# Kernel tuning notes

Hardware: AMD Instinct MI355X
Metric: run time of the kernel (lower is better)

The kernel has to match this reference:

```python
import jax, jax.numpy as jnp
import numpy as np

N, E, H, IN, OUT, A, L = 20000, 320000, 128, 16, 16, 4, 4
EPS = 1e-5


def _ln(x, g, b):
    mu = jnp.mean(x, axis=-1, keepdims=True)
    v = jnp.mean((x - mu) ** 2, axis=-1, keepdims=True)
    return (x - mu) * jax.lax.rsqrt(v + EPS) * g + b


def setup_inputs() -> dict:
    key = jax.random.key(0)
    ks = jax.random.split(key, 24)
    x = jax.random.normal(ks[0], (N, 3), dtype=jnp.float32)
    h = jax.random.normal(ks[1], (N, IN), dtype=jnp.float32)
    src = jax.random.randint(ks[2], (E,), 0, N)
    src = src.at[:N].set(jnp.arange(N))  # ensure every node has out-degree>=1 so c>0
    dst = jax.random.randint(ks[3], (E,), 0, N)
    edges = jnp.stack([src, dst]).astype(jnp.int32)
    edge_attr = jax.random.normal(ks[4], (E, A), dtype=jnp.float32)
    s = 0.05
    d_in = 2 * H + 1 + A
    p = {
        "emb_w": jax.random.normal(ks[5], (IN, H)) * s, "emb_b": jnp.zeros((H,)),
        "out_w": jax.random.normal(ks[6], (H, OUT)) * s, "out_b": jnp.zeros((OUT,)),
        "pe_w1": jax.random.normal(ks[7], (L, d_in, H)) * s, "pe_b1": jnp.zeros((L, H)),
        "pe_g1": jnp.ones((L, H)), "pe_bb1": jnp.zeros((L, H)),
        "pe_w2": jax.random.normal(ks[8], (L, H, H)) * s, "pe_b2": jnp.zeros((L, H)),
        "pe_g2": jnp.ones((L, H)), "pe_bb2": jnp.zeros((L, H)),
        "px_w1": jax.random.normal(ks[9], (L, H, H)) * s, "px_b1": jnp.zeros((L, H)),
        "px_g1": jnp.ones((L, H)), "px_bb1": jnp.zeros((L, H)),
        "px_w2": jax.random.normal(ks[10], (L, H, 1)) * s, "px_b2": jnp.zeros((L, 1)),
        "ph_w1": jax.random.normal(ks[11], (L, 2 * H, H)) * s, "ph_b1": jnp.zeros((L, H)),
        "ph_g1": jnp.ones((L, H)), "ph_bb1": jnp.zeros((L, H)),
        "ph_w2": jax.random.normal(ks[12], (L, H, H)) * s, "ph_b2": jnp.zeros((L, H)),
    }
    out = {"x": x, "h": h, "edges": edges, "edge_attr": edge_attr}
    out.update(p)
    return out


def reference(x, h, edges, edge_attr, emb_w, emb_b, out_w, out_b,
              pe_w1, pe_b1, pe_g1, pe_bb1, pe_w2, pe_b2, pe_g2, pe_bb2,
              px_w1, px_b1, px_g1, px_bb1, px_w2, px_b2,
              ph_w1, ph_b1, ph_g1, ph_bb1, ph_w2, ph_b2):
    n = x.shape[0]
    j, i = edges[0], edges[1]  # PyG: x_j = source, x_i = target; aggregate at target i
    # c = in-neighborhood size computed from edge_index[0] (as in the original code)
    c = jax.ops.segment_sum(jnp.ones((edges.shape[1],), x.dtype), j, num_segments=n)[:, None]
    h = h @ emb_w + emb_b
    for l in range(L):
        d = x[i] - x[j]                                   # [E,3]
        d2 = jnp.sum(d * d, axis=-1, keepdims=True)       # ||x_i - x_j||^2
        m_in = jnp.concatenate([h[i], h[j], d2, edge_attr], axis=-1)
        t = jax.nn.silu(_ln(m_in @ pe_w1[l] + pe_b1[l], pe_g1[l], pe_bb1[l]))
        mh = jax.nn.silu(_ln(t @ pe_w2[l] + pe_b2[l], pe_g2[l], pe_bb2[l]))  # [E,H]
        t2 = jax.nn.silu(_ln(mh @ px_w1[l] + px_b1[l], px_g1[l], px_bb1[l]))
        mx = d * (t2 @ px_w2[l] + px_b2[l])               # [E,3]
        agg_x = jax.ops.segment_sum(mx, i, num_segments=n)
        agg_h = jax.ops.segment_sum(mh, i, num_segments=n)
        u = jnp.concatenate([h, agg_h], axis=-1)
        t3 = jax.nn.silu(_ln(u @ ph_w1[l] + ph_b1[l], ph_g1[l], ph_bb1[l]))
        h = t3 @ ph_w2[l] + ph_b2[l] + h                  # ResWrapper residual
        x = x + agg_x / c
    h = h @ out_w + out_b
    return (x, h)
```

## Files before the change

kernel.cpp:

```cpp
#include <hip/hip_runtime.h>
#include <hip/hip_bf16.h>

#define NN 20000
#define NE 320000
#define HD 128
#define IND 16
#define OUTD 16
#define NL 4
#define LN_EPS 1e-5f
#define LDA 136

typedef __attribute__((ext_vector_type(8))) short bf16x8;
typedef __attribute__((ext_vector_type(4))) float f32x4;

__device__ __forceinline__ unsigned short f2b(float f) {
  __hip_bfloat16 h = __float2bfloat16(f);
  unsigned short u;
  __builtin_memcpy(&u, &h, 2);
  return u;
}
__device__ __forceinline__ float b2f(unsigned int lo16) {
  union { unsigned int u; float f; } v; v.u = lo16 << 16; return v.f;
}


__global__ void prep_zero_k(const float* __restrict__ xin, float* __restrict__ xf,
                            float* __restrict__ cnt, int* __restrict__ deg) {
  int i = blockIdx.x * 256 + threadIdx.x;
  if (i < NN * 3) xf[i] = xin[i];
  if (i < NN) { cnt[i] = 0.f; deg[i] = 0; }
}

__global__ void count_k(const int* __restrict__ edges, float* __restrict__ cnt,
                        int* __restrict__ deg) {
  int e = blockIdx.x * 256 + threadIdx.x;
  if (e < NE) {
    atomicAdd(&cnt[edges[e]], 1.f);
    atomicAdd(&deg[edges[NE + e]], 1);
  }
}

__global__ void inv_k(float* __restrict__ cnt) {
  int n = blockIdx.x * 256 + threadIdx.x;
  if (n < NN) { float c = cnt[n]; cnt[n] = (c > 0.f) ? 1.f / c : 0.f; }
}

__global__ void scan_k(const int* __restrict__ deg, int* __restrict__ rowptr,
                       int* __restrict__ cursor) {
  __shared__ int part[256];
  const int tid = threadIdx.x;
  const int base = tid * 79;
  int s = 0;
  for (int t = 0; t < 79; ++t) { int idx = base + t; if (idx < NN) s += deg[idx]; }
  part[tid] = s;
  __syncthreads();
  for (int off = 1; off < 256; off <<= 1) {
    int v = (tid >= off) ? part[tid - off] : 0;
    __syncthreads();
    part[tid] += v;
    __syncthreads();
  }
  int run = (tid == 0) ? 0 : part[tid - 1];
  for (int t = 0; t < 79; ++t) {
    int idx = base + t;
    if (idx < NN) { rowptr[idx] = run; cursor[idx] = run; run += deg[idx]; }
  }
  if (tid == 255) rowptr[NN] = run;
}

__global__ void scatter_k(const int* __restrict__ edges, int* __restrict__ cursor,
                          int* __restrict__ eids) {
  int e = blockIdx.x * 256 + threadIdx.x;
  if (e < NE) {
    int d = edges[NE + e];
    int pos = atomicAdd(&cursor[d], 1);
    eids[pos] = e;
  }
}

__global__ void prep_w_k(const float* __restrict__ src, unsigned short* __restrict__ dst,
                         int KT, int Kreal) {
  int i = blockIdx.x * 256 + threadIdx.x;
  int total = NL * KT * 4096;
  if (i >= total) return;
  int kk = i & 31;
  int c = (i >> 5) & 127;
  int lkt = i >> 12;
  int kt = lkt % KT;
  int l = lkt / KT;
  int k = kt * 32 + kk;
  float v = (k < Kreal) ? src[((size_t)l * Kreal + k) * HD + c] : 0.f;
  dst[i] = f2b(v);
}

__global__ void emb_k(const float* __restrict__ hin, const float* __restrict__ w,
                      const float* __restrict__ b, float* __restrict__ hf,
                      unsigned short* __restrict__ hb) {
  int i = blockIdx.x * 256 + threadIdx.x;
  if (i >= NN * HD) return;
  int n = i >> 7, c = i & 127;
  float acc = b[c];
#pragma unroll
  for (int k = 0; k < IND; ++k) acc += hin[n * IND + k] * w[k * HD + c];
  hf[i] = acc;
  hb[i] = f2b(acc);
}

__global__ void prepd_k(const float* __restrict__ xf, const int* __restrict__ edges,
                        const float* __restrict__ ea, float* __restrict__ dvec,
                        unsigned short* __restrict__ e8) {
  int e = blockIdx.x * 256 + threadIdx.x;
  if (e >= NE) return;
  int j = edges[e], i = edges[NE + e];
  float dx = xf[i * 3 + 0] - xf[j * 3 + 0];
  float dy = xf[i * 3 + 1] - xf[j * 3 + 1];
  float dz = xf[i * 3 + 2] - xf[j * 3 + 2];
  float d2 = dx * dx + dy * dy + dz * dz;
  dvec[e * 4 + 0] = dx; dvec[e * 4 + 1] = dy; dvec[e * 4 + 2] = dz; dvec[e * 4 + 3] = d2;
  e8[e * 8 + 0] = f2b(d2);
#pragma unroll
  for (int a = 0; a < 4; ++a) e8[e * 8 + 1 + a] = f2b(ea[e * 4 + a]);
  e8[e * 8 + 5] = 0; e8[e * 8 + 6] = 0; e8[e * 8 + 7] = 0;
}

__global__ void outproj_k(const float* __restrict__ hf, const float* __restrict__ w,
                          const float* __restrict__ b, float* __restrict__ out) {
  int i = blockIdx.x * 256 + threadIdx.x;
  if (i >= NN * OUTD) return;
  int n = i >> 4, o = i & 15;
  float acc = b[o];
#pragma unroll 8
  for (int k = 0; k < HD; ++k) acc += hf[(size_t)n * HD + k] * w[k * OUTD + o];
  out[NN * 3 + i] = acc;
}

__global__ void xcopy_k(const float* __restrict__ xf, float* __restrict__ out) {
  int i = blockIdx.x * 256 + threadIdx.x;
  if (i < NN * 3) out[i] = xf[i];
}


__global__ __launch_bounds__(256) void gather_k(const unsigned short* __restrict__ tbuf,
                                                const float* __restrict__ sc,
                                                const float* __restrict__ dvec,
                                                const int* __restrict__ rowptr,
                                                const int* __restrict__ eids,
                                                const float* __restrict__ cinv,
                                                unsigned short* __restrict__ agghb,
                                                float* __restrict__ xf) {
  const int n = blockIdx.x * 4 + (threadIdx.x >> 6);
  if (n >= NN) return;
  const int lane = threadIdx.x & 63;
  const int s = rowptr[n], e = rowptr[n + 1];
  float a0 = 0.f, a1 = 0.f, xa = 0.f;
  for (int t = s; t < e; ++t) {
    const int eid = eids[t];
    const unsigned int v = *(const unsigned int*)(tbuf + (size_t)eid * HD + lane * 2);
    a0 += b2f(v & 0xffffu);
    a1 += b2f(v >> 16);
    if (lane < 3) xa += dvec[(size_t)eid * 4 + lane] * sc[eid];
  }
  const unsigned int pk = (unsigned int)f2b(a0) | ((unsigned int)f2b(a1) << 16);
  *(unsigned int*)(agghb + (size_t)n * HD + lane * 2) = pk;
  if (lane < 3) xf[n * 3 + lane] += xa * cinv[n];
}


__device__ __forceinline__ void mfma_w(const bf16x8 (&A)[2], const bf16x8 (&B)[8],
                                       f32x4 (&acc)[2][8]) {
#pragma unroll
  for (int mf = 0; mf < 2; ++mf)
#pragma unroll
    for (int nf = 0; nf < 8; ++nf)
      acc[mf][nf] = __builtin_amdgcn_mfma_f32_16x16x32_bf16(A[mf], B[nf], acc[mf][nf], 0, 0, 0);
}

#define ZACC()                                          \
  _Pragma("unroll") for (int a_ = 0; a_ < 2; ++a_)      \
  _Pragma("unroll") for (int b_ = 0; b_ < 8; ++b_)      \
      acc[a_][b_] = (f32x4){0.f, 0.f, 0.f, 0.f}

#define GEMM_PIPE(NKT, LD)                              \
  LD(0, A0, B0);                                        \
  _Pragma("unroll") for (int kt = 0; kt < (NKT); ++kt) {\
    if ((kt & 1) == 0) {                                \
      if (kt + 1 < (NKT)) LD(kt + 1, A1, B1);           \
      mfma_w(A0, B0, acc);                              \
    } else {                                            \
      if (kt + 1 < (NKT)) LD(kt + 1, A0, B0);           \
      mfma_w(A1, B1, acc);                              \
    }                                                   \
  }

__device__ __forceinline__ void ln_silu_w(f32x4 (&acc)[2][8], const float* bias,
                                          const float* g, const float* bb, int lid) {
  float biasc[8], gc[8], bbc[8];
#pragma unroll
  for (int nf = 0; nf < 8; ++nf) {
    const int c = nf * 16 + lid;
    biasc[nf] = bias[c]; gc[nf] = g[c]; bbc[nf] = bb[c];
  }
#pragma unroll
  for (int mf = 0; mf < 2; ++mf)
#pragma unroll
    for (int nf = 0; nf < 8; ++nf)
#pragma unroll
      for (int rg = 0; rg < 4; ++rg) acc[mf][nf][rg] += biasc[nf];

  float s_[2][4], ss_[2][4];
#pragma unroll
  for (int mf = 0; mf < 2; ++mf)
#pragma unroll
    for (int rg = 0; rg < 4; ++rg) {
      float a = 0.f, b = 0.f;
#pragma unroll
      for (int nf = 0; nf < 8; ++nf) { float v = acc[mf][nf][rg]; a += v; b += v * v; }
      s_[mf][rg] = a; ss_[mf][rg] = b;
    }
#pragma unroll
  for (int m = 1; m < 16; m <<= 1) {
#pragma unroll
    for (int mf = 0; mf < 2; ++mf)
#pragma unroll
      for (int rg = 0; rg < 4; ++rg) {
        s_[mf][rg] += __shfl_xor(s_[mf][rg], m);
        ss_[mf][rg] += __shfl_xor(ss_[mf][rg], m);
      }
  }
#pragma unroll
  for (int mf = 0; mf < 2; ++mf)
#pragma unroll
    for (int rg = 0; rg < 4; ++rg) {
      const float mu = s_[mf][rg] * (1.f / HD);
      const float var = ss_[mf][rg] * (1.f / HD) - mu * mu;
      const float rstd = rsqrtf(var + LN_EPS);
#pragma unroll
      for (int nf = 0; nf < 8; ++nf) {
        float v = acc[mf][nf][rg];
        v = (v - mu) * rstd * gc[nf] + bbc[nf];
        acc[mf][nf][rg] = v / (1.f + __expf(-v));
      }
    }
}

__device__ __forceinline__ void write_strip(const f32x4 (&acc)[2][8], unsigned short* At,
                                            int rbase, int lid, int q) {
#pragma unroll
  for (int mf = 0; mf < 2; ++mf)
#pragma unroll
    for (int rg = 0; rg < 4; ++rg) {
      const int row = rbase + mf * 16 + q * 4 + rg;
#pragma unroll
      for (int nf = 0; nf < 8; ++nf)
        At[row * LDA + nf * 16 + lid] = f2b(acc[mf][nf][rg]);
    }
}


struct EP {
  const unsigned short* hb;
  const unsigned short* e8;
  const int* edges;
  const unsigned short *w1, *w2, *w3;
  const float *b1, *g1, *bb1, *b2, *g2, *bb2, *b3, *g3, *bb3;
  const float *w4, *b4;
  unsigned short* tbuf;
  float* sc;
};

__global__ __launch_bounds__(256, 3) void edge_k(EP p) {
  __shared__ __align__(16) unsigned short At[128 * LDA];

  const int tid = threadIdx.x, lane = tid & 63, lid = lane & 15, q = lane >> 4;
  const int wave = tid >> 6;
  const int rbase = wave * 32;
  const int row0 = blockIdx.x * 128;

  int ei[2], ej[2];
#pragma unroll
  for (int mf = 0; mf < 2; ++mf) {
    const int r = row0 + rbase + mf * 16 + lid;
    ei[mf] = p.edges[NE + r];
    ej[mf] = p.edges[r];
  }

  const bf16x8 zv = {0, 0, 0, 0, 0, 0, 0, 0};

  auto LD1 = [&](int kt, bf16x8 (&A)[2], bf16x8 (&B)[8]) {
#pragma unroll
    for (int mf = 0; mf < 2; ++mf) {
      if (kt < 4)
        A[mf] = *(const bf16x8*)(p.hb + (size_t)ei[mf] * HD + kt * 32 + q * 8);
      else if (kt < 8)
        A[mf] = *(const bf16x8*)(p.hb + (size_t)ej[mf] * HD + (kt - 4) * 32 + q * 8);
      else if (q == 0)
        A[mf] = *(const bf16x8*)(p.e8 + (size_t)(row0 + rbase + mf * 16 + lid) * 8);
      else
        A[mf] = zv;
    }
#pragma unroll
    for (int nf = 0; nf < 8; ++nf)
      B[nf] = *(const bf16x8*)(p.w1 + (size_t)kt * 4096 + (nf * 16 + lid) * 32 + q * 8);
  };
  auto LDW = [&](const unsigned short* wt, int kt, bf16x8 (&A)[2], bf16x8 (&B)[8]) {
#pragma unroll
    for (int mf = 0; mf < 2; ++mf)
      A[mf] = *(const bf16x8*)&At[(rbase + mf * 16 + lid) * LDA + kt * 32 + q * 8];
#pragma unroll
    for (int nf = 0; nf < 8; ++nf)
      B[nf] = *(const bf16x8*)(wt + (size_t)kt * 4096 + (nf * 16 + lid) * 32 + q * 8);
  };
  auto LD2 = [&](int kt, bf16x8 (&A)[2], bf16x8 (&B)[8]) { LDW(p.w2, kt, A, B); };
  auto LD3 = [&](int kt, bf16x8 (&A)[2], bf16x8 (&B)[8]) { LDW(p.w3, kt, A, B); };

  f32x4 acc[2][8];
  bf16x8 A0[2], B0[8], A1[2], B1[8];

  ZACC();
  GEMM_PIPE(9, LD1);
  ln_silu_w(acc, p.b1, p.g1, p.bb1, lid);
  write_strip(acc, At, rbase, lid, q);

  ZACC();
  GEMM_PIPE(4, LD2);
  ln_silu_w(acc, p.b2, p.g2, p.bb2, lid);
  write_strip(acc, At, rbase, lid, q);

#pragma unroll
  for (int it = 0; it < 8; ++it) {
    const int idx = it * 64 + lane;
    const int row = idx >> 4, sl = idx & 15;
    const uint4 v = *(const uint4*)&At[(rbase + row) * LDA + sl * 8];
    *(uint4*)(p.tbuf + (size_t)(row0 + rbase + row) * HD + sl * 8) = v;
  }

  ZACC();
  GEMM_PIPE(4, LD3);
  ln_silu_w(acc, p.b3, p.g3, p.bb3, lid);

  float w4c[8];
#pragma unroll
  for (int nf = 0; nf < 8; ++nf) w4c[nf] = p.w4[nf * 16 + lid];
  float dp[2][4];
#pragma unroll
  for (int mf = 0; mf < 2; ++mf)
#pragma unroll
    for (int rg = 0; rg < 4; ++rg) {
      float a = 0.f;
#pragma unroll
      for (int nf = 0; nf < 8; ++nf) a += acc[mf][nf][rg] * w4c[nf];
      dp[mf][rg] = a;
    }
#pragma unroll
  for (int m = 1; m < 16; m <<= 1) {
#pragma unroll
    for (int mf = 0; mf < 2; ++mf)
#pragma unroll
      for (int rg = 0; rg < 4; ++rg) dp[mf][rg] += __shfl_xor(dp[mf][rg], m);
  }
  if (lid == 0) {
    const float b4 = p.b4[0];
#pragma unroll
    for (int mf = 0; mf < 2; ++mf)
#pragma unroll
      for (int rg = 0; rg < 4; ++rg)
        p.sc[row0 + rbase + mf * 16 + q * 4 + rg] = dp[mf][rg] + b4;
  }
}


struct NP {
  const float* hf;
  const unsigned short* hb;
  const unsigned short* agghb;
  const unsigned short *w4t, *w5t;
  const float *b1, *g1, *bb1, *b5;
  float* hf_out;
  unsigned short* hb_out;
};

__global__ __launch_bounds__(128, 3) void node_k(NP p) {
  __shared__ __align__(16) unsigned short At[64 * LDA];

  const int tid = threadIdx.x, lane = tid & 63, lid = lane & 15, q = lane >> 4;
  const int wave = tid >> 6;
  const int rbase = wave * 32;
  const int row0 = blockIdx.x * 64;

  int nrow[2];
  bool okm[2];
#pragma unroll
  for (int mf = 0; mf < 2; ++mf) {
    nrow[mf] = row0 + rbase + mf * 16 + lid;
    okm[mf] = nrow[mf] < NN;
  }

  const bf16x8 zv = {0, 0, 0, 0, 0, 0, 0, 0};

  auto LD4 = [&](int kt, bf16x8 (&A)[2], bf16x8 (&B)[8]) {
#pragma unroll
    for (int mf = 0; mf < 2; ++mf) {
      if (!okm[mf]) { A[mf] = zv; continue; }
      const unsigned short* s = (kt < 4)
          ? (p.hb + (size_t)nrow[mf] * HD + kt * 32 + q * 8)
          : (p.agghb + (size_t)nrow[mf] * HD + (kt - 4) * 32 + q * 8);
      A[mf] = *(const bf16x8*)s;
    }
#pragma unroll
    for (int nf = 0; nf < 8; ++nf)
      B[nf] = *(const bf16x8*)(p.w4t + (size_t)kt * 4096 + (nf * 16 + lid) * 32 + q * 8);
  };
  auto LD5 = [&](int kt, bf16x8 (&A)[2], bf16x8 (&B)[8]) {
#pragma unroll
    for (int mf = 0; mf < 2; ++mf)
      A[mf] = *(const bf16x8*)&At[(rbase + mf * 16 + lid) * LDA + kt * 32 + q * 8];
#pragma unroll
    for (int nf = 0; nf < 8; ++nf)
      B[nf] = *(const bf16x8*)(p.w5t + (size_t)kt * 4096 + (nf * 16 + lid) * 32 + q * 8);
  };

  f32x4 acc[2][8];
  bf16x8 A0[2], B0[8], A1[2], B1[8];

  ZACC();
  GEMM_PIPE(8, LD4);
  ln_silu_w(acc, p.b1, p.g1, p.bb1, lid);
  write_strip(acc, At, rbase, lid, q);

  ZACC();
  GEMM_PIPE(4, LD5);

  float biasc[8];
#pragma unroll
  for (int nf = 0; nf < 8; ++nf) biasc[nf] = p.b5[nf * 16 + lid];
#pragma unroll
  for (int mf = 0; mf < 2; ++mf)
#pragma unroll
    for (int rg = 0; rg < 4; ++rg) {
      const int n = row0 + rbase + mf * 16 + q * 4 + rg;
      if (n < NN) {
#pragma unroll
        for (int nf = 0; nf < 8; ++nf) {
          const int c = nf * 16 + lid;
          const float v = acc[mf][nf][rg] + biasc[nf] + p.hf[(size_t)n * HD + c];
          p.hf_out[(size_t)n * HD + c] = v;
          p.hb_out[(size_t)n * HD + c] = f2b(v);
        }
      }
    }
}


extern "C" void kernel_launch(void* const* d_in, const int* in_sizes, int n_in,
                              void* d_out, int out_size, void* d_ws, size_t ws_size,
                              hipStream_t stream) {
  (void)in_sizes; (void)n_in; (void)out_size; (void)ws_size;
  const float* x_in = (const float*)d_in[0];
  const float* h_in = (const float*)d_in[1];
  const int* edges = (const int*)d_in[2];
  const float* eattr = (const float*)d_in[3];
  const float* emb_w = (const float*)d_in[4];
  const float* emb_b = (const float*)d_in[5];
  const float* out_w = (const float*)d_in[6];
  const float* out_b = (const float*)d_in[7];
  const float* pe_w1 = (const float*)d_in[8];
  const float* pe_b1 = (const float*)d_in[9];
  const float* pe_g1 = (const float*)d_in[10];
  const float* pe_bb1 = (const float*)d_in[11];
  const float* pe_w2 = (const float*)d_in[12];
  const float* pe_b2 = (const float*)d_in[13];
  const float* pe_g2 = (const float*)d_in[14];
  const float* pe_bb2 = (const float*)d_in[15];
  const float* px_w1 = (const float*)d_in[16];
  const float* px_b1 = (const float*)d_in[17];
  const float* px_g1 = (const float*)d_in[18];
  const float* px_bb1 = (const float*)d_in[19];
  const float* px_w2 = (const float*)d_in[20];
  const float* px_b2 = (const float*)d_in[21];
  const float* ph_w1 = (const float*)d_in[22];
  const float* ph_b1 = (const float*)d_in[23];
  const float* ph_g1 = (const float*)d_in[24];
  const float* ph_bb1 = (const float*)d_in[25];
  const float* ph_w2 = (const float*)d_in[26];
  const float* ph_b2 = (const float*)d_in[27];
  float* out = (float*)d_out;

  char* ws = (char*)d_ws;
  size_t off = 0;
  auto alloc = [&](size_t bytes) -> void* {
    void* ptr = ws + off;
    off = (off + bytes + 255) & ~(size_t)255;
    return ptr;
  };
  float* hf = (float*)alloc((size_t)NN * HD * 4);
  unsigned short* hb = (unsigned short*)alloc((size_t)NN * HD * 2);
  unsigned short* agghb = (unsigned short*)alloc((size_t)NN * HD * 2);
  float* xf = (float*)alloc((size_t)NN * 3 * 4);
  float* cinv = (float*)alloc((size_t)NN * 4);
  float* dvec = (float*)alloc((size_t)NE * 4 * 4);
  unsigned short* e8 = (unsigned short*)alloc((size_t)NE * 8 * 2);
  unsigned short* tbuf = (unsigned short*)alloc((size_t)NE * HD * 2);
  float* sc = (float*)alloc((size_t)NE * 4);
  int* deg = (int*)alloc((size_t)NN * 4);
  int* cursor = (int*)alloc((size_t)NN * 4);
  int* rowptr = (int*)alloc((size_t)(NN + 1) * 4);
  int* eids = (int*)alloc((size_t)NE * 4);
  unsigned short* w1t = (unsigned short*)alloc((size_t)NL * 9 * 4096 * 2);
  unsigned short* w2t = (unsigned short*)alloc((size_t)NL * 4 * 4096 * 2);
  unsigned short* w3t = (unsigned short*)alloc((size_t)NL * 4 * 4096 * 2);
  unsigned short* w4t = (unsigned short*)alloc((size_t)NL * 8 * 4096 * 2);
  unsigned short* w5t = (unsigned short*)alloc((size_t)NL * 4 * 4096 * 2);

  prep_zero_k<<<(NN * 3 + 255) / 256, 256, 0, stream>>>(x_in, xf, cinv, deg);
  count_k<<<(NE + 255) / 256, 256, 0, stream>>>(edges, cinv, deg);
  inv_k<<<(NN + 255) / 256, 256, 0, stream>>>(cinv);
  scan_k<<<1, 256, 0, stream>>>(deg, rowptr, cursor);
  scatter_k<<<(NE + 255) / 256, 256, 0, stream>>>(edges, cursor, eids);
  prep_w_k<<<(NL * 9 * 4096 + 255) / 256, 256, 0, stream>>>(pe_w1, w1t, 9, 261);
  prep_w_k<<<(NL * 4 * 4096 + 255) / 256, 256, 0, stream>>>(pe_w2, w2t, 4, 128);
  prep_w_k<<<(NL * 4 * 4096 + 255) / 256, 256, 0, stream>>>(px_w1, w3t, 4, 128);
  prep_w_k<<<(NL * 8 * 4096 + 255) / 256, 256, 0, stream>>>(ph_w1, w4t, 8, 256);
  prep_w_k<<<(NL * 4 * 4096 + 255) / 256, 256, 0, stream>>>(ph_w2, w5t, 4, 128);
  emb_k<<<(NN * HD + 255) / 256, 256, 0, stream>>>(h_in, emb_w, emb_b, hf, hb);

  const int egrid = NE / 128;
  const int ngrid = (NN + 63) / 64;

  for (int l = 0; l < NL; ++l) {
    prepd_k<<<(NE + 255) / 256, 256, 0, stream>>>(xf, edges, eattr, dvec, e8);
    {
      EP p{};
      p.hb = hb; p.e8 = e8; p.edges = edges;
      p.w1 = w1t + (size_t)l * 9 * 4096;
      p.w2 = w2t + (size_t)l * 4 * 4096;
      p.w3 = w3t + (size_t)l * 4 * 4096;
      p.b1 = pe_b1 + l * HD; p.g1 = pe_g1 + l * HD; p.bb1 = pe_bb1 + l * HD;
      p.b2 = pe_b2 + l * HD; p.g2 = pe_g2 + l * HD; p.bb2 = pe_bb2 + l * HD;
      p.b3 = px_b1 + l * HD; p.g3 = px_g1 + l * HD; p.bb3 = px_bb1 + l * HD;
      p.w4 = px_w2 + l * HD; p.b4 = px_b2 + l;
      p.tbuf = tbuf; p.sc = sc;
      edge_k<<<egrid, 256, 0, stream>>>(p);
    }
    gather_k<<<(NN + 3) / 4, 256, 0, stream>>>(tbuf, sc, dvec, rowptr, eids, cinv, agghb, xf);
    {
      NP p{};
      p.hf = hf; p.hb = hb; p.agghb = agghb;
      p.w4t = w4t + (size_t)l * 8 * 4096;
      p.w5t = w5t + (size_t)l * 4 * 4096;
      p.b1 = ph_b1 + l * HD; p.g1 = ph_g1 + l * HD; p.bb1 = ph_bb1 + l * HD;
      p.b5 = ph_b2 + l * HD;
      p.hf_out = hf; p.hb_out = hb;
      node_k<<<ngrid, 128, 0, stream>>>(p);
    }
  }

  outproj_k<<<(NN * OUTD + 255) / 256, 256, 0, stream>>>(hf, out_w, out_b, out);
  xcopy_k<<<(NN * 3 + 255) / 256, 256, 0, stream>>>(xf, out);
}
```

Baseline: 1.228 ms.

## Fuse per-edge geometry prep into edge kernel and precompute mx for gather

Removes the per-layer prepd_k kernel by computing the edge distance and the bf16 edge features inside the edge MLP kernel's A-fragment load. The edge kernel now writes the final mx = d*scale (3 floats per edge) instead of the scalar scale, so gather reads one array rather than dvec and sc. The gather loop is unrolled by four with split accumulators to expose more memory parallelism. The five weight-prep launches are merged into one. This saves one launch and the dvec/e8 traffic per layer, at the cost of redundant x reads inside the edge kernel and a wave-local shared-memory staging of the scale.

After: 1.185 ms. 3.4% less time.

```diff
diff --git a/kernel.cpp b/kernel.cpp
--- a/kernel.cpp
+++ b/kernel.cpp
@@ -78,19 +78,26 @@
   }
 }
 
-__global__ void prep_w_k(const float* __restrict__ src, unsigned short* __restrict__ dst,
-                         int KT, int Kreal) {
+__global__ void prep_w_all_k(const float* __restrict__ pe_w1, const float* __restrict__ pe_w2,
+                             const float* __restrict__ px_w1, const float* __restrict__ ph_w1,
+                             const float* __restrict__ ph_w2,
+                             unsigned short* __restrict__ w1t, unsigned short* __restrict__ w2t,
+                             unsigned short* __restrict__ w3t, unsigned short* __restrict__ w4t,
+                             unsigned short* __restrict__ w5t) {
+  const int G1 = NL * 9 * 4096, G2 = G1 + NL * 4 * 4096, G3 = G2 + NL * 4 * 4096,
+            G4 = G3 + NL * 8 * 4096, G5 = G4 + NL * 4 * 4096;
   int i = blockIdx.x * 256 + threadIdx.x;
-  int total = NL * KT * 4096;
-  if (i >= total) return;
-  int kk = i & 31;
-  int c = (i >> 5) & 127;
-  int lkt = i >> 12;
-  int kt = lkt % KT;
-  int l = lkt / KT;
-  int k = kt * 32 + kk;
-  float v = (k < Kreal) ? src[((size_t)l * Kreal + k) * HD + c] : 0.f;
-  dst[i] = f2b(v);
+  const float* src; unsigned short* dst; int KT, Kreal, li;
+  if (i < G1)      { src = pe_w1; dst = w1t; KT = 9; Kreal = 261; li = i; }
+  else if (i < G2) { src = pe_w2; dst = w2t; KT = 4; Kreal = 128; li = i - G1; }
+  else if (i < G3) { src = px_w1; dst = w3t; KT = 4; Kreal = 128; li = i - G2; }
+  else if (i < G4) { src = ph_w1; dst = w4t; KT = 8; Kreal = 256; li = i - G3; }
+  else if (i < G5) { src = ph_w2; dst = w5t; KT = 4; Kreal = 128; li = i - G4; }
+  else return;
+  const int kk = li & 31, c = (li >> 5) & 127, lkt = li >> 12;
+  const int kt = lkt % KT, l = lkt / KT, k = kt * 32 + kk;
+  const float v = (k < Kreal) ? src[((size_t)l * Kreal + k) * HD + c] : 0.f;
+  dst[li] = f2b(v);
 }
 
 __global__ void emb_k(const float* __restrict__ hin, const float* __restrict__ w,
@@ -104,23 +111,6 @@
   for (int k = 0; k < IND; ++k) acc += hin[n * IND + k] * w[k * HD + c];
   hf[i] = acc;
   hb[i] = f2b(acc);
-}
-
-__global__ void prepd_k(const float* __restrict__ xf, const int* __restrict__ edges,
-                        const float* __restrict__ ea, float* __restrict__ dvec,
-                        unsigned short* __restrict__ e8) {
-  int e = blockIdx.x * 256 + threadIdx.x;
-  if (e >= NE) return;
-  int j = edges[e], i = edges[NE + e];
-  float dx = xf[i * 3 + 0] - xf[j * 3 + 0];
-  float dy = xf[i * 3 + 1] - xf[j * 3 + 1];
-  float dz = xf[i * 3 + 2] - xf[j * 3 + 2];
-  float d2 = dx * dx + dy * dy + dz * dz;
-  dvec[e * 4 + 0] = dx; dvec[e * 4 + 1] = dy; dvec[e * 4 + 2] = dz; dvec[e * 4 + 3] = d2;
-  e8[e * 8 + 0] = f2b(d2);
-#pragma unroll
-  for (int a = 0; a < 4; ++a) e8[e * 8 + 1 + a] = f2b(ea[e * 4 + a]);
-  e8[e * 8 + 5] = 0; e8[e * 8 + 6] = 0; e8[e * 8 + 7] = 0;
 }
 
 __global__ void outproj_k(const float* __restrict__ hf, const float* __restrict__ w,
@@ -141,8 +131,7 @@
 
 
 __global__ __launch_bounds__(256) void gather_k(const unsigned short* __restrict__ tbuf,
-                                                const float* __restrict__ sc,
-                                                const float* __restrict__ dvec,
+                                                const float* __restrict__ mx,
                                                 const int* __restrict__ rowptr,
                                                 const int* __restrict__ eids,
                                                 const float* __restrict__ cinv,
@@ -152,14 +141,31 @@
   if (n >= NN) return;
   const int lane = threadIdx.x & 63;
   const int s = rowptr[n], e = rowptr[n + 1];
-  float a0 = 0.f, a1 = 0.f, xa = 0.f;
-  for (int t = s; t < e; ++t) {
+  float a0 = 0.f, a1 = 0.f, b0 = 0.f, b1 = 0.f, xa = 0.f, xb = 0.f;
+  int t = s;
+  for (; t + 4 <= e; t += 4) {
+    const int e0 = eids[t], e1 = eids[t + 1], e2 = eids[t + 2], e3 = eids[t + 3];
+    const unsigned int v0 = *(const unsigned int*)(tbuf + (size_t)e0 * HD + lane * 2);
+    const unsigned int v1 = *(const unsigned int*)(tbuf + (size_t)e1 * HD + lane * 2);
+    const unsigned int v2 = *(const unsigned int*)(tbuf + (size_t)e2 * HD + lane * 2);
+    const unsigned int v3 = *(const unsigned int*)(tbuf + (size_t)e3 * HD + lane * 2);
+    a0 += b2f(v0 & 0xffffu) + b2f(v1 & 0xffffu);
+    b0 += b2f(v2 & 0xffffu) + b2f(v3 & 0xffffu);
+    a1 += b2f(v0 >> 16) + b2f(v1 >> 16);
+    b1 += b2f(v2 >> 16) + b2f(v3 >> 16);
+    if (lane < 3) {
+      xa += mx[(size_t)e0 * 3 + lane] + mx[(size_t)e1 * 3 + lane];
+      xb += mx[(size_t)e2 * 3 + lane] + mx[(size_t)e3 * 3 + lane];
+    }
+  }
+  for (; t < e; ++t) {
     const int eid = eids[t];
     const unsigned int v = *(const unsigned int*)(tbuf + (size_t)eid * HD + lane * 2);
     a0 += b2f(v & 0xffffu);
     a1 += b2f(v >> 16);
-    if (lane < 3) xa += dvec[(size_t)eid * 4 + lane] * sc[eid];
-  }
+    if (lane < 3) xa += mx[(size_t)eid * 3 + lane];
+  }
+  a0 += b0; a1 += b1; xa += xb;
   const unsigned int pk = (unsigned int)f2b(a0) | ((unsigned int)f2b(a1) << 16);
   *(unsigned int*)(agghb + (size_t)n * HD + lane * 2) = pk;
   if (lane < 3) xf[n * 3 + lane] += xa * cinv[n];
@@ -259,17 +265,19 @@
 
 struct EP {
   const unsigned short* hb;
-  const unsigned short* e8;
+  const float* xf;
+  const float* ea;
   const int* edges;
   const unsigned short *w1, *w2, *w3;
   const float *b1, *g1, *bb1, *b2, *g2, *bb2, *b3, *g3, *bb3;
   const float *w4, *b4;
   unsigned short* tbuf;
-  float* sc;
+  float* mx;
 };
 
 __global__ __launch_bounds__(256, 3) void edge_k(EP p) {
   __shared__ __align__(16) unsigned short At[128 * LDA];
+  __shared__ float scSh[4][32];
 
   const int tid = threadIdx.x, lane = tid & 63, lid = lane & 15, q = lane >> 4;
   const int wave = tid >> 6;
@@ -293,9 +301,16 @@
         A[mf] = *(const bf16x8*)(p.hb + (size_t)ei[mf] * HD + kt * 32 + q * 8);
       else if (kt < 8)
         A[mf] = *(const bf16x8*)(p.hb + (size_t)ej[mf] * HD + (kt - 4) * 32 + q * 8);
-      else if (q == 0)
-        A[mf] = *(const bf16x8*)(p.e8 + (size_t)(row0 + rbase + mf * 16 + lid) * 8);
-      else
+      else if (q == 0) {
+        const int e_ = row0 + rbase + mf * 16 + lid;
+        const float* xi = p.xf + (size_t)ei[mf] * 3;
+        const float* xj = p.xf + (size_t)ej[mf] * 3;
+        const float dx = xi[0] - xj[0], dy = xi[1] - xj[1], dz = xi[2] - xj[2];
+        const float d2 = dx * dx + dy * dy + dz * dz;
+        const float4 eav = *(const float4*)(p.ea + (size_t)e_ * 4);
+        unsigned short t_[8] = {f2b(d2), f2b(eav.x), f2b(eav.y), f2b(eav.z), f2b(eav.w), 0, 0, 0};
+        A[mf] = *(const bf16x8*)t_;
+      } else
         A[mf] = zv;
     }
 #pragma unroll
@@ -364,7 +379,20 @@
     for (int mf = 0; mf < 2; ++mf)
 #pragma unroll
       for (int rg = 0; rg < 4; ++rg)
-        p.sc[row0 + rbase + mf * 16 + q * 4 + rg] = dp[mf][rg] + b4;
+        scSh[wave][mf * 16 + q * 4 + rg] = dp[mf][rg] + b4;
+  }
+  asm volatile("" ::: "memory");
+  if (q == 0) {
+#pragma unroll
+    for (int mf = 0; mf < 2; ++mf) {
+      const int e_ = row0 + rbase + mf * 16 + lid;
+      const float scv = scSh[wave][mf * 16 + lid];
+      const float* xi = p.xf + (size_t)ei[mf] * 3;
+      const float* xj = p.xf + (size_t)ej[mf] * 3;
+      p.mx[(size_t)e_ * 3 + 0] = (xi[0] - xj[0]) * scv;
+      p.mx[(size_t)e_ * 3 + 1] = (xi[1] - xj[1]) * scv;
+      p.mx[(size_t)e_ * 3 + 2] = (xi[2] - xj[2]) * scv;
+    }
   }
 }
 
@@ -497,10 +525,8 @@
   unsigned short* agghb = (unsigned short*)alloc((size_t)NN * HD * 2);
   float* xf = (float*)alloc((size_t)NN * 3 * 4);
   float* cinv = (float*)alloc((size_t)NN * 4);
-  float* dvec = (float*)alloc((size_t)NE * 4 * 4);
-  unsigned short* e8 = (unsigned short*)alloc((size_t)NE * 8 * 2);
   unsigned short* tbuf = (unsigned short*)alloc((size_t)NE * HD * 2);
-  float* sc = (float*)alloc((size_t)NE * 4);
+  float* mx = (float*)alloc((size_t)NE * 3 * 4);
   int* deg = (int*)alloc((size_t)NN * 4);
   int* cursor = (int*)alloc((size_t)NN * 4);
   int* rowptr = (int*)alloc((size_t)(NN + 1) * 4);
@@ -516,21 +542,20 @@
   inv_k<<<(NN + 255) / 256, 256, 0, stream>>>(cinv);
   scan_k<<<1, 256, 0, stream>>>(deg, rowptr, cursor);
   scatter_k<<<(NE + 255) / 256, 256, 0, stream>>>(edges, cursor, eids);
-  prep_w_k<<<(NL * 9 * 4096 + 255) / 256, 256, 0, stream>>>(pe_w1, w1t, 9, 261);
-  prep_w_k<<<(NL * 4 * 4096 + 255) / 256, 256, 0, stream>>>(pe_w2, w2t, 4, 128);
-  prep_w_k<<<(NL * 4 * 4096 + 255) / 256, 256, 0, stream>>>(px_w1, w3t, 4, 128);
-  prep_w_k<<<(NL * 8 * 4096 + 255) / 256, 256, 0, stream>>>(ph_w1, w4t, 8, 256);
-  prep_w_k<<<(NL * 4 * 4096 + 255) / 256, 256, 0, stream>>>(ph_w2, w5t, 4, 128);
+  {
+    const int total = NL * (9 + 4 + 4 + 8 + 4) * 4096;
+    prep_w_all_k<<<(total + 255) / 256, 256, 0, stream>>>(pe_w1, pe_w2, px_w1, ph_w1, ph_w2,
+                                                          w1t, w2t, w3t, w4t, w5t);
+  }
   emb_k<<<(NN * HD + 255) / 256, 256, 0, stream>>>(h_in, emb_w, emb_b, hf, hb);
 
   const int egrid = NE / 128;
   const int ngrid = (NN + 63) / 64;
 
   for (int l = 0; l < NL; ++l) {
-    prepd_k<<<(NE + 255) / 256, 256, 0, stream>>>(xf, edges, eattr, dvec, e8);
     {
       EP p{};
-      p.hb = hb; p.e8 = e8; p.edges = edges;
+      p.hb = hb; p.xf = xf; p.ea = eattr; p.edges = edges;
       p.w1 = w1t + (size_t)l * 9 * 4096;
       p.w2 = w2t + (size_t)l * 4 * 4096;
       p.w3 = w3t + (size_t)l * 4 * 4096;
@@ -538,10 +563,10 @@
       p.b2 = pe_b2 + l * HD; p.g2 = pe_g2 + l * HD; p.bb2 = pe_bb2 + l * HD;
       p.b3 = px_b1 + l * HD; p.g3 = px_g1 + l * HD; p.bb3 = px_bb1 + l * HD;
       p.w4 = px_w2 + l * HD; p.b4 = px_b2 + l;
-      p.tbuf = tbuf; p.sc = sc;
+      p.tbuf = tbuf; p.mx = mx;
       edge_k<<<egrid, 256, 0, stream>>>(p);
     }
-    gather_k<<<(NN + 3) / 4, 256, 0, stream>>>(tbuf, sc, dvec, rowptr, eids, cinv, agghb, xf);
+    gather_k<<<(NN + 3) / 4, 256, 0, stream>>>(tbuf, mx, rowptr, eids, cinv, agghb, xf);
     {
       NP p{};
       p.hf = hf; p.hb = hb; p.agghb = agghb;
```
